# Performance work log

Measured on AMD Instinct MI355X. Metric: run time of the kernel, lower is better.

## Reference

```python
import jax, jax.numpy as jnp
import numpy as np

T, B, H, L = 128, 64, 1024, 4


def setup_inputs() -> dict:
    key = jax.random.key(0)
    k1, k2, k3 = jax.random.split(key, 3)
    inputs = jax.random.normal(k1, (T, B, H), dtype=jnp.float32)
    W = jax.random.normal(k2, (L, H, 4 * H), dtype=jnp.float32) * 0.02
    U = jax.random.normal(k3, (L, H, 4 * H), dtype=jnp.float32) * 0.02
    b = jnp.zeros((L, 4 * H), dtype=jnp.float32)
    return {"inputs": inputs, "W": W, "U": U, "b": b}


def _lstm_cell(x, h_prev, c_prev, Wj, Uj, bj):
    # Standard keras LSTMCell math: z = x@W + h@U + b, gates order i,f,g,o
    z = x @ Wj + h_prev @ Uj + bj  # [B, 4H]
    i, f, g, o = jnp.split(z, 4, axis=-1)
    c = jax.nn.sigmoid(f) * c_prev + jax.nn.sigmoid(i) * jnp.tanh(g)
    h = jax.nn.sigmoid(o) * jnp.tanh(c)
    return h, c


def reference(inputs, W, U, b):
    n_layers = W.shape[0]
    batch = inputs.shape[1]
    hidden = W.shape[1]
    # state_c in the original holds hidden states (a), state_h holds cell states (bb)
    a0 = jnp.zeros((n_layers, batch, hidden), dtype=inputs.dtype)
    b0 = jnp.zeros((n_layers, batch, hidden), dtype=inputs.dtype)

    def step(carry, x):
        a, bb = carry
        cur = x
        for j in range(n_layers):  # static, small layer loop
            # original passes (c, h) to keras cell -> h_tm1 = a[j], c_tm1 = bb[j]
            h, c = _lstm_cell(cur, a[j], bb[j], W[j], U[j], b[j])
            a = a.at[j].set(h)
            bb = bb.at[j].set(c)
            cur = c  # original feeds the new CELL state to the next layer
        return (a, bb), None

    (a, bb), _ = jax.lax.scan(step, (a0, b0), inputs)
    # original returns state_h.read(num_layers-1) == final cell state of last layer
    return bb[n_layers - 1]
```

## Files before the change

kernel.cpp:

```cpp
#include <hip/hip_runtime.h>

#define TT 128
#define BB 64
#define HH 1024
#define LL 4
#define NWG 256
#define NPROD 64u

typedef _Float16 f16;
typedef __attribute__((ext_vector_type(4))) _Float16 f16x4;
typedef __attribute__((ext_vector_type(8))) _Float16 f16x8;
typedef __attribute__((ext_vector_type(4))) float f32x4;
typedef unsigned long long u64;

__device__ __align__(16) f16 g_in16[TT][65536];
__device__ __align__(16) f16 g_c16[LL][TT + 1][65536];
__device__ __align__(16) f16 g_h16[LL][TT + 1][65536];
__device__ __align__(16) float g_c32[LL][BB][HH];
__device__ unsigned g_done[LL][TT];

__global__ void k_init() {
  unsigned tid = blockIdx.x * blockDim.x + threadIdx.x;
  unsigned n = gridDim.x * blockDim.x;
  float* c32 = &g_c32[0][0][0];
  for (unsigned i = tid; i < LL * BB * HH; i += n) c32[i] = 0.f;
  for (unsigned i = tid; i < LL * 65536 / 2; i += n) {
    int jj = i >> 15, q = i & 32767;
    ((unsigned*)&g_h16[jj][0][0])[q] = 0u;
  }
  unsigned* pd = &g_done[0][0];
  for (unsigned i = tid; i < LL * TT; i += n) pd[i] = 0u;
}

__global__ void k_pack_in(const float* __restrict__ inp) {
  int tid = blockIdx.x * blockDim.x + threadIdx.x;
  int t = tid >> 14, q = tid & 16383;
  int row = q >> 8, hu = (q & 255) << 2;
  const float4 x = *(const float4*)(inp + ((size_t)t << 16) + (row << 10) + hu);
  int rg = row >> 4, ktp = hu >> 5;
  int ln = (((hu >> 2) & 3) << 4) | (row & 15);
  int e0 = ((hu >> 4) & 1) << 2;
  f16x4 v = {(f16)x.x, (f16)x.y, (f16)x.z, (f16)x.w};
  *(f16x4*)&g_in16[t][(((rg * 32 + ktp) * 64 + ln) << 3) + e0] = v;
}

__device__ __forceinline__ float sigf(float x) { return 1.f / (1.f + __expf(-x)); }
__device__ __forceinline__ float tanh_(float x) {
  float q = __expf(-2.f * fabsf(x));
  return copysignf((1.f - q) / (1.f + q), x);
}
__device__ __forceinline__ f16x4 lo8(f16x8 v) { return __builtin_shufflevector(v, v, 0, 1, 2, 3); }
__device__ __forceinline__ f16x4 hi8(f16x8 v) { return __builtin_shufflevector(v, v, 4, 5, 6, 7); }
__device__ __forceinline__ void waitflag(const unsigned* p, unsigned n) {
  while (__hip_atomic_load(p, __ATOMIC_RELAXED, __HIP_MEMORY_SCOPE_AGENT) < n)
    __builtin_amdgcn_s_sleep(2);
}
__device__ __forceinline__ f16x8 ldA(const f16* p, bool coh) {
  if (coh) {
    const u64* q = (const u64*)p;
    union { u64 v[2]; f16x8 h; } u;
    u.v[0] = __hip_atomic_load(q,     __ATOMIC_RELAXED, __HIP_MEMORY_SCOPE_AGENT);
    u.v[1] = __hip_atomic_load(q + 1, __ATOMIC_RELAXED, __HIP_MEMORY_SCOPE_AGENT);
    return u.h;
  }
  return *(const f16x8*)p;
}

#define MFMA16(A_, B_, C_) __builtin_amdgcn_mfma_f32_16x16x16f16(A_, B_, C_, 0, 0, 0)

__global__ __launch_bounds__(512, 2) void k_main(const float* __restrict__ W,
                                                 const float* __restrict__ U,
                                                 const float* __restrict__ bias,
                                                 float* __restrict__ out) {
  const int j = blockIdx.x >> 6, s = blockIdx.x & 63;
  const int tid = threadIdx.x, lane = tid & 63, wv = tid >> 6;
  const int mat = wv >> 2, kq = wv & 3;
  __shared__ float zl[16384];

  const float* src = (mat ? U : W) + (size_t)j * (HH * 4 * HH);
  const int colb = s * 16 + (lane & 15);
  const int kb0 = kq * 256 + ((lane >> 4) << 2);
  f16x8 Wr[32];
#pragma unroll
  for (int kk = 0; kk < 16; ++kk)
#pragma unroll
    for (int cfp = 0; cfp < 2; ++cfp) {
      f16x8 v;
#pragma unroll
      for (int hf = 0; hf < 2; ++hf)
#pragma unroll
        for (int e = 0; e < 4; ++e)
          v[hf * 4 + e] = (f16)src[(size_t)(kb0 + kk * 16 + e) * 4096 + (cfp * 2 + hf) * 1024 + colb];
      Wr[kk * 2 + cfp] = v;
    }

  const int row = tid >> 3, hl0 = (tid & 7) * 2;
  const int hu0 = s * 16 + hl0;
  float br[2][4];
#pragma unroll
  for (int el = 0; el < 2; ++el)
#pragma unroll
    for (int g = 0; g < 4; ++g) br[el][g] = bias[j * 4096 + g * 1024 + hu0 + el];
  const int fibase = ((((row >> 4) * 32 + (hu0 >> 5)) * 64 +
                       ((((hu0 >> 2) & 3) << 4) | (row & 15))) << 3) +
                     ((((hu0 >> 4) & 1) << 2) | (hu0 & 3));
  const int fib2 = fibase >> 1;
  unsigned* const hPub = (unsigned*)&g_h16[j][0][0];
  unsigned* const cPub = (unsigned*)&g_c16[j][0][0];
  float* c32p = &g_c32[j][row][hu0];
  const int ktp0 = kq * 8;
  const bool coh = mat || (j > 0);

  for (int t = 0; t < TT; ++t) {
    if (tid == 0) {
      if (j > 0) waitflag(&g_done[j - 1][t], NPROD);
      if (t > 0) waitflag(&g_done[j][t - 1], NPROD);
    }
    __syncthreads();
    asm volatile("" ::: "memory");

    const f16* Ab = mat ? &g_h16[j][t][0]
                        : (j ? &g_c16[j - 1][t + 1][0] : &g_in16[t][0]);
    f16x8 a[2][4];
#pragma unroll
    for (int rf = 0; rf < 4; ++rf)
      a[0][rf] = ldA(Ab + (rf * 32 + ktp0) * 512 + lane * 8, coh);

    f32x4 acc[4][4];
#pragma unroll
    for (int rf = 0; rf < 4; ++rf)
#pragma unroll
      for (int cf = 0; cf < 4; ++cf) acc[rf][cf] = (f32x4){0.f, 0.f, 0.f, 0.f};

#pragma unroll
    for (int kc = 0; kc < 8; ++kc) {
      if (kc < 7) {
#pragma unroll
        for (int rf = 0; rf < 4; ++rf)
          a[(kc + 1) & 1][rf] = ldA(Ab + (rf * 32 + ktp0 + kc + 1) * 512 + lane * 8, coh);
      }
#pragma unroll
      for (int hf = 0; hf < 2; ++hf) {
        f16x4 a4[4];
#pragma unroll
        for (int rf = 0; rf < 4; ++rf)
          a4[rf] = hf ? hi8(a[kc & 1][rf]) : lo8(a[kc & 1][rf]);
#pragma unroll
        for (int cf = 0; cf < 4; ++cf) {
          const f16x8 wreg = Wr[(kc * 2 + hf) * 2 + (cf >> 1)];
          const f16x4 b4 = (cf & 1) ? hi8(wreg) : lo8(wreg);
#pragma unroll
          for (int rf = 0; rf < 4; ++rf) acc[rf][cf] = MFMA16(a4[rf], b4, acc[rf][cf]);
        }
      }
    }

    float gsum[2][4];
#pragma unroll
    for (int P = 0; P < 2; ++P) {
      __syncthreads();
#pragma unroll
      for (int rf = 0; rf < 4; ++rf)
#pragma unroll
        for (int ch = 0; ch < 2; ++ch) {
          const int cf = P * 2 + ch;
#pragma unroll
          for (int ri = 0; ri < 4; ++ri) {
            const int rr = rf * 16 + ((lane >> 4) << 2) + ri;
            const int c2 = ch * 16 + (lane & 15);
            zl[wv * 2048 + rr * 32 + (c2 ^ ((rr & 4) << 2))] = acc[rf][cf][ri];
          }
        }
      __syncthreads();
#pragma unroll
      for (int ch = 0; ch < 2; ++ch) {
        const int idx = row * 32 + ((ch * 16 + hl0) ^ ((row & 4) << 2));
        float sx = 0.f, sy = 0.f;
#pragma unroll
        for (int w = 0; w < 8; ++w) {
          const float2 v = *(const float2*)&zl[w * 2048 + idx];
          sx += v.x; sy += v.y;
        }
        gsum[0][P * 2 + ch] = sx;
        gsum[1][P * 2 + ch] = sy;
      }
    }

    float cns[2], hns[2];
#pragma unroll
    for (int el = 0; el < 2; ++el) {
      const float zi = gsum[el][0] + br[el][0];
      const float zf = gsum[el][1] + br[el][1];
      const float zg = gsum[el][2] + br[el][2];
      const float zo = gsum[el][3] + br[el][3];
      const float cp = c32p[el];
      const float cn = sigf(zf) * cp + sigf(zi) * tanh_(zg);
      c32p[el] = cn;
      cns[el] = cn;
      hns[el] = sigf(zo) * tanh_(cn);
    }
    {
      union { f16 h[2]; unsigned u; } ph, pc;
      ph.h[0] = (f16)hns[0]; ph.h[1] = (f16)hns[1];
      __hip_atomic_store(hPub + (size_t)(t + 1) * 32768 + fib2, ph.u,
                         __ATOMIC_RELAXED, __HIP_MEMORY_SCOPE_AGENT);
      if (j < 3) {
        pc.h[0] = (f16)cns[0]; pc.h[1] = (f16)cns[1];
        __hip_atomic_store(cPub + (size_t)(t + 1) * 32768 + fib2, pc.u,
                           __ATOMIC_RELAXED, __HIP_MEMORY_SCOPE_AGENT);
      }
      if (j == 3 && t == TT - 1) {
        out[(row << 10) + hu0] = cns[0];
        out[(row << 10) + hu0 + 1] = cns[1];
      }
    }

    asm volatile("s_waitcnt vmcnt(0)" ::: "memory");
    __syncthreads();
    if (tid == 0)
      __hip_atomic_fetch_add(&g_done[j][t], 1u, __ATOMIC_RELAXED, __HIP_MEMORY_SCOPE_AGENT);
  }
}

extern "C" void kernel_launch(void* const* d_in, const int* in_sizes, int n_in,
                              void* d_out, int out_size, void* d_ws, size_t ws_size,
                              hipStream_t stream) {
  const float* inp  = (const float*)d_in[0];
  const float* W    = (const float*)d_in[1];
  const float* U    = (const float*)d_in[2];
  const float* bias = (const float*)d_in[3];
  float* out = (float*)d_out;
  k_init<<<256, 256, 0, stream>>>();
  k_pack_in<<<4096, 512, 0, stream>>>(inp);
  k_main<<<NWG, 512, 0, stream>>>(W, U, bias, out);
}
```

Before: 2.490 ms.

## Replace per-step counter barrier with per-producer epoch flags waited per wave

The single global done-counter per (layer, step) is replaced by one epoch flag per producer workgroup. Each workgroup now stores its step number to its own flag instead of doing an atomic add. Each wave polls, with a wave-wide vote, only the 16 producer flags covering its own K slice. This drops the thread-0 wait plus block barrier at the top of each step, so input and recurrent waves can start as soon as their own data is ready. The LDS reduction swizzle also gains an extra XOR term to cut bank conflicts. The cost is more polling traffic from many lanes.

Measured after the change: 2.634 ms. 5.8% more time.

```diff
diff --git a/kernel.cpp b/kernel.cpp
--- a/kernel.cpp
+++ b/kernel.cpp
@@ -5,7 +5,6 @@
 #define HH 1024
 #define LL 4
 #define NWG 256
-#define NPROD 64u
 
 typedef _Float16 f16;
 typedef __attribute__((ext_vector_type(4))) _Float16 f16x4;
@@ -17,7 +16,7 @@
 __device__ __align__(16) f16 g_c16[LL][TT + 1][65536];
 __device__ __align__(16) f16 g_h16[LL][TT + 1][65536];
 __device__ __align__(16) float g_c32[LL][BB][HH];
-__device__ unsigned g_done[LL][TT];
+__device__ unsigned g_ep[LL][64];
 
 __global__ void k_init() {
   unsigned tid = blockIdx.x * blockDim.x + threadIdx.x;
@@ -28,8 +27,8 @@
     int jj = i >> 15, q = i & 32767;
     ((unsigned*)&g_h16[jj][0][0])[q] = 0u;
   }
-  unsigned* pd = &g_done[0][0];
-  for (unsigned i = tid; i < LL * TT; i += n) pd[i] = 0u;
+  unsigned* pe = &g_ep[0][0];
+  for (unsigned i = tid; i < LL * 64; i += n) pe[i] = 0u;
 }
 
 __global__ void k_pack_in(const float* __restrict__ inp) {
@@ -51,9 +50,12 @@
 }
 __device__ __forceinline__ f16x4 lo8(f16x8 v) { return __builtin_shufflevector(v, v, 0, 1, 2, 3); }
 __device__ __forceinline__ f16x4 hi8(f16x8 v) { return __builtin_shufflevector(v, v, 4, 5, 6, 7); }
-__device__ __forceinline__ void waitflag(const unsigned* p, unsigned n) {
-  while (__hip_atomic_load(p, __ATOMIC_RELAXED, __HIP_MEMORY_SCOPE_AGENT) < n)
-    __builtin_amdgcn_s_sleep(2);
+__device__ __forceinline__ void waitep(const unsigned* ep, unsigned target) {
+  for (;;) {
+    unsigned e = __hip_atomic_load(ep, __ATOMIC_RELAXED, __HIP_MEMORY_SCOPE_AGENT);
+    if (__all((int)(e >= target))) break;
+    __builtin_amdgcn_s_sleep(1);
+  }
 }
 __device__ __forceinline__ f16x8 ldA(const f16* p, bool coh) {
   if (coh) {
@@ -67,6 +69,7 @@
 }
 
 #define MFMA16(A_, B_, C_) __builtin_amdgcn_mfma_f32_16x16x16f16(A_, B_, C_, 0, 0, 0)
+#define SWZ(r) ((((r) & 4) << 2) ^ (((r) & 3) << 3))
 
 __global__ __launch_bounds__(512, 2) void k_main(const float* __restrict__ W,
                                                  const float* __restrict__ U,
@@ -110,13 +113,15 @@
   float* c32p = &g_c32[j][row][hu0];
   const int ktp0 = kq * 8;
   const bool coh = mat || (j > 0);
+  const unsigned* epX = (j > 0) ? &g_ep[j - 1][kq * 16 + (lane & 15)] : nullptr;
+  const unsigned* epH = &g_ep[j][kq * 16 + (lane & 15)];
 
   for (int t = 0; t < TT; ++t) {
-    if (tid == 0) {
-      if (j > 0) waitflag(&g_done[j - 1][t], NPROD);
-      if (t > 0) waitflag(&g_done[j][t - 1], NPROD);
-    }
-    __syncthreads();
+    if (mat == 0) {
+      if (j > 0) waitep(epX, (unsigned)(t + 1));
+    } else {
+      if (t > 0) waitep(epH, (unsigned)t);
+    }
     asm volatile("" ::: "memory");
 
     const f16* Ab = mat ? &g_h16[j][t][0]
@@ -168,13 +173,13 @@
           for (int ri = 0; ri < 4; ++ri) {
             const int rr = rf * 16 + ((lane >> 4) << 2) + ri;
             const int c2 = ch * 16 + (lane & 15);
-            zl[wv * 2048 + rr * 32 + (c2 ^ ((rr & 4) << 2))] = acc[rf][cf][ri];
+            zl[wv * 2048 + rr * 32 + (c2 ^ SWZ(rr))] = acc[rf][cf][ri];
           }
         }
       __syncthreads();
 #pragma unroll
       for (int ch = 0; ch < 2; ++ch) {
-        const int idx = row * 32 + ((ch * 16 + hl0) ^ ((row & 4) << 2));
+        const int idx = row * 32 + ((ch * 16 + hl0) ^ SWZ(row));
         float sx = 0.f, sy = 0.f;
 #pragma unroll
         for (int w = 0; w < 8; ++w) {
@@ -218,7 +223,8 @@
     asm volatile("s_waitcnt vmcnt(0)" ::: "memory");
     __syncthreads();
     if (tid == 0)
-      __hip_atomic_fetch_add(&g_done[j][t], 1u, __ATOMIC_RELAXED, __HIP_MEMORY_SCOPE_AGENT);
+      __hip_atomic_store(&g_ep[j][s], (unsigned)(t + 1),
+                         __ATOMIC_RELAXED, __HIP_MEMORY_SCOPE_AGENT);
   }
 }
 
```
